# Performance work log

Hardware: AMD Instinct MI355X
Metric: run time of the kernel (lower is better)

Reference implementation:

```python
import jax, jax.numpy as jnp
import numpy as np

DIM = 768
N_HEADS = 12
HEAD_DIM = DIM // N_HEADS

def setup_inputs() -> dict:
    key = jax.random.key(0)
    ks = jax.random.split(key, 5)
    B, N = 8, 1024
    s = 0.02
    x = jax.random.normal(ks[0], (B, N, DIM), dtype=jnp.float32)
    W_qkv = jax.random.normal(ks[1], (DIM, 3 * DIM), dtype=jnp.float32) * s
    b_qkv = jnp.zeros((3 * DIM,), dtype=jnp.float32)
    W_proj = jax.random.normal(ks[2], (DIM, DIM), dtype=jnp.float32) * s
    b_proj = jnp.zeros((DIM,), dtype=jnp.float32)
    return {"x": x, "W_qkv": W_qkv, "b_qkv": b_qkv, "W_proj": W_proj, "b_proj": b_proj}

def reference(x, W_qkv, b_qkv, W_proj, b_proj):
    B, N, D = x.shape
    qkv = x @ W_qkv + b_qkv                                   # [B,N,3D]
    qkv = qkv.reshape(B, N, 3, N_HEADS, HEAD_DIM)
    q, k, v = qkv[:, :, 0], qkv[:, :, 1], qkv[:, :, 2]        # [B,N,H,hd]
    q = q.transpose(0, 2, 1, 3)                               # [B,H,N,hd]
    k = k.transpose(0, 2, 1, 3)
    v = v.transpose(0, 2, 1, 3)
    scores = jnp.einsum('bhqd,bhkd->bhqk', q, k) / jnp.sqrt(jnp.float32(HEAD_DIM))
    attn = jax.nn.softmax(scores, axis=-1)
    out = jnp.einsum('bhqk,bhkd->bhqd', attn, v)              # [B,H,N,hd]
    out = out.transpose(0, 2, 1, 3).reshape(B, N, D)
    return out @ W_proj + b_proj
```

## Files before the change

kernel.cpp:

```cpp
#include <hip/hip_runtime.h>
#include <hip/hip_bf16.h>


typedef __bf16 bf16x8 __attribute__((ext_vector_type(8)));
typedef float f32x4 __attribute__((ext_vector_type(4)));

#define MFMA16(a, b, c) __builtin_amdgcn_mfma_f32_16x16x32_bf16(a, b, c, 0, 0, 0)

#if defined(__has_builtin) && __has_builtin(__builtin_amdgcn_exp2f)
#define EXP2(x) __builtin_amdgcn_exp2f(x)
#else
#define EXP2(x) exp2f(x)
#endif

__device__ inline __bf16 to_bf16(float f) {
  __hip_bfloat16 h = __float2bfloat16(f);
  return *reinterpret_cast<__bf16*>(&h);
}

__device__ __forceinline__ void gload16(const void* g, void* l) {
  __builtin_amdgcn_global_load_lds(
      (const __attribute__((address_space(1))) unsigned int*)(unsigned long long)g,
      (__attribute__((address_space(3))) unsigned int*)(unsigned long long)l,
      16, 0, 0);
}

__global__ void ws_diag_kernel(float* out, int n, float val) {
  int i = blockIdx.x * 256 + threadIdx.x;
  if (i < n) out[i] = val;
}

__global__ __launch_bounds__(256) void convert_x_kernel(
    const float* __restrict__ x, __hip_bfloat16* __restrict__ xc, int n8) {
  int i = blockIdx.x * 256 + threadIdx.x;
  if (i >= n8) return;
  float4 a = ((const float4*)x)[i * 2], b = ((const float4*)x)[i * 2 + 1];
  __hip_bfloat16 o[8] = {__float2bfloat16(a.x), __float2bfloat16(a.y),
                         __float2bfloat16(a.z), __float2bfloat16(a.w),
                         __float2bfloat16(b.x), __float2bfloat16(b.y),
                         __float2bfloat16(b.z), __float2bfloat16(b.w)};
  *(int4*)(xc + (size_t)i * 8) = *(const int4*)o;
}

__global__ void convert_transpose_kernel(const float* __restrict__ W,
                                         __hip_bfloat16* __restrict__ Wt,
                                         int rows, int cols) {
  __shared__ __hip_bfloat16 tile[32][33];
  const int tc = blockIdx.x * 32, tr = blockIdx.y * 32;
  const int tx = threadIdx.x, ty = threadIdx.y;
#pragma unroll
  for (int i = 0; i < 4; ++i) {
    int r = ty + i * 8;
    tile[r][tx] = __float2bfloat16(W[(size_t)(tr + r) * cols + tc + tx]);
  }
  __syncthreads();
#pragma unroll
  for (int i = 0; i < 4; ++i) {
    int r = ty + i * 8;
    Wt[(size_t)(tc + r) * rows + tr + tx] = tile[tx][r];
  }
}

constexpr int GK = 768;

__global__ __launch_bounds__(256) void gemm_qkv_kernel(
    const __hip_bfloat16* __restrict__ A,
    const __hip_bfloat16* __restrict__ Bt,
    const float* __restrict__ bias,
    __hip_bfloat16* __restrict__ Qw,
    __hip_bfloat16* __restrict__ Kw,
    __hip_bfloat16* __restrict__ Vt) {
  __shared__ __align__(16) __bf16 As[128 * 32];
  __shared__ __align__(16) __bf16 Bs[128 * 32];
  const int tid = threadIdx.x;
  const int lane = tid & 63, wave = tid >> 6;
  const int wr = wave >> 1, wc = wave & 1;
  const int m0 = blockIdx.x * 128, n0 = blockIdx.y * 128;
  const int fr = lane & 15, q4 = lane >> 4;

  const int r4 = lane >> 2, c8 = (lane & 3) * 8;
  const __hip_bfloat16* ga0 = A + (size_t)(m0 + wave * 32 + r4) * GK + c8;
  const __hip_bfloat16* gb0 = Bt + (size_t)(n0 + wave * 32 + r4) * GK + c8;
  __bf16* la0 = &As[wave * 1024];
  __bf16* lb0 = &Bs[wave * 1024];

  f32x4 acc[4][4] = {};

  for (int kt = 0; kt < GK / 32; ++kt) {
    __syncthreads();
    gload16(ga0 + kt * 32, la0);
    gload16(ga0 + kt * 32 + 16 * GK, la0 + 512);
    gload16(gb0 + kt * 32, lb0);
    gload16(gb0 + kt * 32 + 16 * GK, lb0 + 512);
    __syncthreads();
    bf16x8 af[4], bfr[4];
#pragma unroll
    for (int i = 0; i < 4; ++i)
      af[i] = *(const bf16x8*)(&As[(wr * 64 + i * 16 + fr) * 32 + q4 * 8]);
#pragma unroll
    for (int j = 0; j < 4; ++j)
      bfr[j] = *(const bf16x8*)(&Bs[(wc * 64 + j * 16 + fr) * 32 + q4 * 8]);
#pragma unroll
    for (int i = 0; i < 4; ++i)
#pragma unroll
      for (int j = 0; j < 4; ++j)
        acc[i][j] = MFMA16(af[i], bfr[j], acc[i][j]);
  }

#pragma unroll
  for (int j = 0; j < 4; ++j) {
    int col = n0 + wc * 64 + j * 16 + fr;
    int which = col / 768;
    int rem = col - which * 768;
    int h = rem >> 6, d = rem & 63;
    float bv = bias[col];
    if (which == 2) {
#pragma unroll
      for (int i = 0; i < 4; ++i) {
        int row0 = m0 + wr * 64 + i * 16 + q4 * 4;
        int bb = row0 >> 10, nn = row0 & 1023;
        __hip_bfloat16 o[4];
#pragma unroll
        for (int r = 0; r < 4; ++r) o[r] = __float2bfloat16(acc[i][j][r] + bv);
        *(int2*)(Vt + (((size_t)(bb * 12 + h)) << 16) + ((size_t)d << 10) + nn) =
            *(const int2*)o;
      }
    } else {
      __hip_bfloat16* dst = (which == 0) ? Qw : Kw;
      float scale = (which == 0) ? 0.18033688011112042f : 1.0f;
#pragma unroll
      for (int i = 0; i < 4; ++i) {
#pragma unroll
        for (int r = 0; r < 4; ++r) {
          int row = m0 + wr * 64 + i * 16 + q4 * 4 + r;
          int bb = row >> 10, nn = row & 1023;
          float v = (acc[i][j][r] + bv) * scale;
          dst[(((size_t)(bb * 12 + h) * 1024 + nn) << 6) + d] = __float2bfloat16(v);
        }
      }
    }
  }
}

__global__ __launch_bounds__(256) void gemm_proj_kernel(
    const __hip_bfloat16* __restrict__ A,
    const __hip_bfloat16* __restrict__ Bt,
    const float* __restrict__ bias,
    float* __restrict__ out) {
  __shared__ __align__(16) __bf16 As[128 * 32];
  __shared__ __align__(16) __bf16 Bs[128 * 32];
  const int tid = threadIdx.x;
  const int lane = tid & 63, wave = tid >> 6;
  const int wr = wave >> 1, wc = wave & 1;
  const int m0 = blockIdx.x * 128, n0 = blockIdx.y * 128;
  const int fr = lane & 15, q4 = lane >> 4;

  const int r4 = lane >> 2, c8 = (lane & 3) * 8;
  const __hip_bfloat16* ga0 = A + (size_t)(m0 + wave * 32 + r4) * GK + c8;
  const __hip_bfloat16* gb0 = Bt + (size_t)(n0 + wave * 32 + r4) * GK + c8;
  __bf16* la0 = &As[wave * 1024];
  __bf16* lb0 = &Bs[wave * 1024];

  f32x4 acc[4][4] = {};

  for (int kt = 0; kt < GK / 32; ++kt) {
    __syncthreads();
    gload16(ga0 + kt * 32, la0);
    gload16(ga0 + kt * 32 + 16 * GK, la0 + 512);
    gload16(gb0 + kt * 32, lb0);
    gload16(gb0 + kt * 32 + 16 * GK, lb0 + 512);
    __syncthreads();
    bf16x8 af[4], bfr[4];
#pragma unroll
    for (int i = 0; i < 4; ++i)
      af[i] = *(const bf16x8*)(&As[(wr * 64 + i * 16 + fr) * 32 + q4 * 8]);
#pragma unroll
    for (int j = 0; j < 4; ++j)
      bfr[j] = *(const bf16x8*)(&Bs[(wc * 64 + j * 16 + fr) * 32 + q4 * 8]);
#pragma unroll
    for (int i = 0; i < 4; ++i)
#pragma unroll
      for (int j = 0; j < 4; ++j)
        acc[i][j] = MFMA16(af[i], bfr[j], acc[i][j]);
  }

#pragma unroll
  for (int j = 0; j < 4; ++j) {
    int col = n0 + wc * 64 + j * 16 + fr;
    float bv = bias[col];
#pragma unroll
    for (int i = 0; i < 4; ++i) {
#pragma unroll
      for (int r = 0; r < 4; ++r) {
        int row = m0 + wr * 64 + i * 16 + q4 * 4 + r;
        out[(size_t)row * 768 + col] = acc[i][j][r] + bv;
      }
    }
  }
}

__global__ __launch_bounds__(512) void attn_kernel(
    const __hip_bfloat16* __restrict__ Qw,
    const __hip_bfloat16* __restrict__ Kw,
    const __hip_bfloat16* __restrict__ Vt,
    __hip_bfloat16* __restrict__ O) {
  constexpr int LP = 72;
  __shared__ __bf16 smem[18432];
  __bf16* Qs = smem;
  __bf16* K1 = smem;
  __bf16* V1 = smem + 4608;
  __bf16* K0 = smem + 9216;
  __bf16* V0 = smem + 13824;
  const int tid = threadIdx.x;
  const int lane = tid & 63, wave = tid >> 6;
  const int fr = lane & 15, q4 = lane >> 4;
  const int bh = blockIdx.x % 96, qt = blockIdx.x / 96;
  const __hip_bfloat16* Qb = Qw + ((size_t)bh * 1024 + qt * 128) * 64;
  const __hip_bfloat16* Kb = Kw + (size_t)bh * 65536;
  const __hip_bfloat16* Vb = Vt + (size_t)bh * 65536;

  const int krow = tid >> 3, kc = (tid & 7) * 8;
  int4 kregA = *(const int4*)(Kb + (size_t)krow * 64 + kc);
  int4 vregA = *(const int4*)(Vb + ((size_t)krow << 10) + kc);

#pragma unroll
  for (int i = 0; i < 2; ++i) {
    int s = tid + 512 * i;
    int row = s >> 3, c = (s & 7) * 8;
    *(int4*)(&Qs[row * LP + c]) = *(const int4*)(Qb + row * 64 + c);
  }
  __syncthreads();
  bf16x8 qf[2];
#pragma unroll
  for (int ks = 0; ks < 2; ++ks)
    qf[ks] = *(const bf16x8*)(&Qs[(wave * 16 + fr) * LP + ks * 32 + q4 * 8]);

  float l_i = 0.f;
  f32x4 accO[4] = {};

  const int sc8 = tid & 7;
  const int sbase = ((sc8 >> 2) << 5) | ((sc8 & 1) << 4) | (((sc8 >> 1) & 1) << 2);

  *(int4*)(&K0[krow * LP + kc]) = kregA;
  *(int2*)(&V0[krow * LP + sbase]) = make_int2(vregA.x, vregA.y);
  *(int2*)(&V0[krow * LP + sbase + 8]) = make_int2(vregA.z, vregA.w);
  int4 kregB = *(const int4*)(Kb + (size_t)(64 + krow) * 64 + kc);
  int4 vregB = *(const int4*)(Vb + ((size_t)krow << 10) + 64 + kc);
  __syncthreads();

  auto compute_tile = [&](const __bf16* Kbuf, const __bf16* Vbuf) {
    f32x4 scT[4];
    __builtin_amdgcn_s_setprio(1);
#pragma unroll
    for (int nt = 0; nt < 4; ++nt) {
      bf16x8 kf0 = *(const bf16x8*)(&Kbuf[(nt * 16 + fr) * LP + q4 * 8]);
      bf16x8 kf1 = *(const bf16x8*)(&Kbuf[(nt * 16 + fr) * LP + 32 + q4 * 8]);
      f32x4 z = {};
      z = MFMA16(kf0, qf[0], z);
      scT[nt] = MFMA16(kf1, qf[1], z);
    }
    __builtin_amdgcn_s_setprio(0);
    float rs = 0.f;
#pragma unroll
    for (int nt = 0; nt < 4; ++nt)
#pragma unroll
      for (int r = 0; r < 4; ++r) {
        float p = EXP2(scT[nt][r]);
        scT[nt][r] = p;
        rs += p;
      }
    l_i += rs;
#pragma unroll
    for (int ks = 0; ks < 2; ++ks) {
      bf16x8 pf;
#pragma unroll
      for (int e = 0; e < 4; ++e) {
        pf[e] = to_bf16(scT[2 * ks][e]);
        pf[4 + e] = to_bf16(scT[2 * ks + 1][e]);
      }
      __builtin_amdgcn_s_setprio(1);
#pragma unroll
      for (int dt = 0; dt < 4; ++dt) {
        bf16x8 vf = *(const bf16x8*)(&Vbuf[(dt * 16 + fr) * LP + ks * 32 + q4 * 8]);
        accO[dt] = MFMA16(pf, vf, accO[dt]);
      }
      __builtin_amdgcn_s_setprio(0);
    }
  };

  for (int kt2 = 0; kt2 < 16; kt2 += 2) {
    compute_tile(K0, V0);
    *(int4*)(&K1[krow * LP + kc]) = kregB;
    *(int2*)(&V1[krow * LP + sbase]) = make_int2(vregB.x, vregB.y);
    *(int2*)(&V1[krow * LP + sbase + 8]) = make_int2(vregB.z, vregB.w);
    if (kt2 + 2 < 16) {
      kregA = *(const int4*)(Kb + (size_t)((kt2 + 2) * 64 + krow) * 64 + kc);
      vregA = *(const int4*)(Vb + ((size_t)krow << 10) + (kt2 + 2) * 64 + kc);
    }
    __syncthreads();
    compute_tile(K1, V1);
    if (kt2 + 2 < 16) {
      *(int4*)(&K0[krow * LP + kc]) = kregA;
      *(int2*)(&V0[krow * LP + sbase]) = make_int2(vregA.x, vregA.y);
      *(int2*)(&V0[krow * LP + sbase + 8]) = make_int2(vregA.z, vregA.w);
      kregB = *(const int4*)(Kb + (size_t)((kt2 + 3) * 64 + krow) * 64 + kc);
      vregB = *(const int4*)(Vb + ((size_t)krow << 10) + (kt2 + 3) * 64 + kc);
      __syncthreads();
    }
  }

  l_i += __shfl_xor(l_i, 16, 64);
  l_i += __shfl_xor(l_i, 32, 64);
  float lrow[4];
#pragma unroll
  for (int r = 0; r < 4; ++r) lrow[r] = __shfl(l_i, q4 * 4 + r, 64);

  const int h = bh % 12, bb = bh / 12;
#pragma unroll
  for (int dt = 0; dt < 4; ++dt)
#pragma unroll
    for (int r = 0; r < 4; ++r) {
      int row = bb * 1024 + qt * 128 + wave * 16 + q4 * 4 + r;
      int col = h * 64 + dt * 16 + fr;
      O[(size_t)row * 768 + col] = __float2bfloat16(accO[dt][r] / lrow[r]);
    }
}

extern "C" void kernel_launch(void* const* d_in, const int* in_sizes, int n_in,
                              void* d_out, int out_size, void* d_ws, size_t ws_size,
                              hipStream_t stream) {
  const float* x     = (const float*)d_in[0];
  const float* Wqkv  = (const float*)d_in[1];
  const float* bqkv  = (const float*)d_in[2];
  const float* Wproj = (const float*)d_in[3];
  const float* bproj = (const float*)d_in[4];
  float* out = (float*)d_out;

  constexpr size_t NEEDED = 55050240;
  if (ws_size < NEEDED) {
    ws_diag_kernel<<<(out_size + 255) / 256, 256, 0, stream>>>(
        out, out_size, (float)(ws_size >> 20));
    return;
  }

  char* ws = (char*)d_ws;
  __hip_bfloat16* WqkvT  = (__hip_bfloat16*)(ws);
  __hip_bfloat16* WprojT = (__hip_bfloat16*)(ws + 3538944);
  __hip_bfloat16* Qw     = (__hip_bfloat16*)(ws + 4718592);
  __hip_bfloat16* Kw     = (__hip_bfloat16*)(ws + 17301504);
  __hip_bfloat16* Vt     = (__hip_bfloat16*)(ws + 29884416);
  __hip_bfloat16* xc     = (__hip_bfloat16*)(ws + 42467328);
  __hip_bfloat16* attnO  = xc;

  convert_x_kernel<<<3072, 256, 0, stream>>>(x, xc, 786432);
  convert_transpose_kernel<<<dim3(72, 24), dim3(32, 8), 0, stream>>>(
      Wqkv, WqkvT, 768, 2304);
  convert_transpose_kernel<<<dim3(24, 24), dim3(32, 8), 0, stream>>>(
      Wproj, WprojT, 768, 768);
  gemm_qkv_kernel<<<dim3(64, 18), 256, 0, stream>>>(xc, WqkvT, bqkv, Qw, Kw, Vt);
  attn_kernel<<<dim3(96 * 8), 512, 0, stream>>>(Qw, Kw, Vt, attnO);
  gemm_proj_kernel<<<dim3(64, 6), 256, 0, stream>>>(attnO, WprojT, bproj, out);
}
```

Before: 190.5 us.

## Merge prep conversions into one launch and transpose V in separate kernel

Folds the x conversion and both weight convert-transposes into a single prep kernel launch that dispatches on block index, removing two launches. The QKV GEMM now writes V row-major like Q and K, and a new LDS-tiled kernel transposes V into the layout the attention kernel reads. This replaces the GEMM's strided 8-byte V stores with coalesced 16-byte stores, at the cost of an extra kernel and an extra pass over V in memory. Workspace buffers are reassigned so Vt reuses the x buffer and the attention output reuses the row-major V buffer.

```diff
diff --git a/kernel.cpp b/kernel.cpp
--- a/kernel.cpp
+++ b/kernel.cpp
@@ -30,24 +30,36 @@
   if (i < n) out[i] = val;
 }
 
-__global__ __launch_bounds__(256) void convert_x_kernel(
-    const float* __restrict__ x, __hip_bfloat16* __restrict__ xc, int n8) {
-  int i = blockIdx.x * 256 + threadIdx.x;
-  if (i >= n8) return;
-  float4 a = ((const float4*)x)[i * 2], b = ((const float4*)x)[i * 2 + 1];
-  __hip_bfloat16 o[8] = {__float2bfloat16(a.x), __float2bfloat16(a.y),
-                         __float2bfloat16(a.z), __float2bfloat16(a.w),
-                         __float2bfloat16(b.x), __float2bfloat16(b.y),
-                         __float2bfloat16(b.z), __float2bfloat16(b.w)};
-  *(int4*)(xc + (size_t)i * 8) = *(const int4*)o;
-}
-
-__global__ void convert_transpose_kernel(const float* __restrict__ W,
-                                         __hip_bfloat16* __restrict__ Wt,
-                                         int rows, int cols) {
+__global__ __launch_bounds__(256) void prep_kernel(
+    const float* __restrict__ x, __hip_bfloat16* __restrict__ xc,
+    const float* __restrict__ Wqkv, __hip_bfloat16* __restrict__ WqkvT,
+    const float* __restrict__ Wproj, __hip_bfloat16* __restrict__ WprojT) {
   __shared__ __hip_bfloat16 tile[32][33];
-  const int tc = blockIdx.x * 32, tr = blockIdx.y * 32;
-  const int tx = threadIdx.x, ty = threadIdx.y;
+  const int b = blockIdx.x;
+  if (b < 3072) {
+    int i = b * 256 + threadIdx.x;
+    float4 a = ((const float4*)x)[i * 2], c = ((const float4*)x)[i * 2 + 1];
+    __hip_bfloat16 o[8] = {__float2bfloat16(a.x), __float2bfloat16(a.y),
+                           __float2bfloat16(a.z), __float2bfloat16(a.w),
+                           __float2bfloat16(c.x), __float2bfloat16(c.y),
+                           __float2bfloat16(c.z), __float2bfloat16(c.w)};
+    *(int4*)(xc + (size_t)i * 8) = *(const int4*)o;
+    return;
+  }
+  const float* W;
+  __hip_bfloat16* Wt;
+  int rows, cols, bx, by;
+  if (b < 4800) {
+    int idx = b - 3072;
+    W = Wqkv; Wt = WqkvT; rows = 768; cols = 2304;
+    bx = idx % 72; by = idx / 72;
+  } else {
+    int idx = b - 4800;
+    W = Wproj; Wt = WprojT; rows = 768; cols = 768;
+    bx = idx % 24; by = idx / 24;
+  }
+  const int tc = bx * 32, tr = by * 32;
+  const int tx = threadIdx.x & 31, ty = threadIdx.x >> 5;
 #pragma unroll
   for (int i = 0; i < 4; ++i) {
     int r = ty + i * 8;
@@ -58,6 +70,33 @@
   for (int i = 0; i < 4; ++i) {
     int r = ty + i * 8;
     Wt[(size_t)(tc + r) * rows + tr + tx] = tile[tx][r];
+  }
+}
+
+__global__ __launch_bounds__(256) void vtrans_kernel(
+    const __hip_bfloat16* __restrict__ Vrow, __hip_bfloat16* __restrict__ Vt) {
+  constexpr int LP = 72;
+  __shared__ __bf16 tile[64 * LP];
+  const int tid = threadIdx.x;
+  const int bh = blockIdx.x;
+  const int n0 = blockIdx.y * 64;
+  const size_t base = (size_t)bh << 16;
+#pragma unroll
+  for (int i = 0; i < 2; ++i) {
+    int s = tid + 256 * i;
+    int r = s >> 3, c8 = (s & 7) * 8;
+    *(int4*)(&tile[r * LP + c8]) =
+        *(const int4*)(Vrow + base + (size_t)(n0 + r) * 64 + c8);
+  }
+  __syncthreads();
+#pragma unroll
+  for (int i = 0; i < 2; ++i) {
+    int s = tid + 256 * i;
+    int d = s >> 3, n8 = (s & 7) * 8;
+    __bf16 o[8];
+#pragma unroll
+    for (int j = 0; j < 8; ++j) o[j] = tile[(n8 + j) * LP + d];
+    *(int4*)(Vt + base + ((size_t)d << 10) + n0 + n8) = *(const int4*)o;
   }
 }
 
@@ -69,7 +108,7 @@
     const float* __restrict__ bias,
     __hip_bfloat16* __restrict__ Qw,
     __hip_bfloat16* __restrict__ Kw,
-    __hip_bfloat16* __restrict__ Vt) {
+    __hip_bfloat16* __restrict__ Vw) {
   __shared__ __align__(16) __bf16 As[128 * 32];
   __shared__ __align__(16) __bf16 Bs[128 * 32];
   const int tid = threadIdx.x;
@@ -114,29 +153,16 @@
     int rem = col - which * 768;
     int h = rem >> 6, d = rem & 63;
     float bv = bias[col];
-    if (which == 2) {
-#pragma unroll
-      for (int i = 0; i < 4; ++i) {
-        int row0 = m0 + wr * 64 + i * 16 + q4 * 4;
-        int bb = row0 >> 10, nn = row0 & 1023;
-        __hip_bfloat16 o[4];
-#pragma unroll
-        for (int r = 0; r < 4; ++r) o[r] = __float2bfloat16(acc[i][j][r] + bv);
-        *(int2*)(Vt + (((size_t)(bb * 12 + h)) << 16) + ((size_t)d << 10) + nn) =
-            *(const int2*)o;
-      }
-    } else {
-      __hip_bfloat16* dst = (which == 0) ? Qw : Kw;
-      float scale = (which == 0) ? 0.18033688011112042f : 1.0f;
-#pragma unroll
-      for (int i = 0; i < 4; ++i) {
-#pragma unroll
-        for (int r = 0; r < 4; ++r) {
-          int row = m0 + wr * 64 + i * 16 + q4 * 4 + r;
-          int bb = row >> 10, nn = row & 1023;
-          float v = (acc[i][j][r] + bv) * scale;
-          dst[(((size_t)(bb * 12 + h) * 1024 + nn) << 6) + d] = __float2bfloat16(v);
-        }
+    __hip_bfloat16* dst = (which == 0) ? Qw : (which == 1) ? Kw : Vw;
+    float scale = (which == 0) ? 0.18033688011112042f : 1.0f;
+#pragma unroll
+    for (int i = 0; i < 4; ++i) {
+#pragma unroll
+      for (int r = 0; r < 4; ++r) {
+        int row = m0 + wr * 64 + i * 16 + q4 * 4 + r;
+        int bb = row >> 10, nn = row & 1023;
+        float v = (acc[i][j][r] + bv) * scale;
+        dst[(((size_t)(bb * 12 + h) * 1024 + nn) << 6) + d] = __float2bfloat16(v);
       }
     }
   }
@@ -348,16 +374,14 @@
   __hip_bfloat16* WprojT = (__hip_bfloat16*)(ws + 3538944);
   __hip_bfloat16* Qw     = (__hip_bfloat16*)(ws + 4718592);
   __hip_bfloat16* Kw     = (__hip_bfloat16*)(ws + 17301504);
-  __hip_bfloat16* Vt     = (__hip_bfloat16*)(ws + 29884416);
+  __hip_bfloat16* Vrow   = (__hip_bfloat16*)(ws + 29884416);
   __hip_bfloat16* xc     = (__hip_bfloat16*)(ws + 42467328);
-  __hip_bfloat16* attnO  = xc;
-
-  convert_x_kernel<<<3072, 256, 0, stream>>>(x, xc, 786432);
-  convert_transpose_kernel<<<dim3(72, 24), dim3(32, 8), 0, stream>>>(
-      Wqkv, WqkvT, 768, 2304);
-  convert_transpose_kernel<<<dim3(24, 24), dim3(32, 8), 0, stream>>>(
-      Wproj, WprojT, 768, 768);
-  gemm_qkv_kernel<<<dim3(64, 18), 256, 0, stream>>>(xc, WqkvT, bqkv, Qw, Kw, Vt);
+  __hip_bfloat16* Vt     = xc;
+  __hip_bfloat16* attnO  = Vrow;
+
+  prep_kernel<<<5376, 256, 0, stream>>>(x, xc, Wqkv, WqkvT, Wproj, WprojT);
+  gemm_qkv_kernel<<<dim3(64, 18), 256, 0, stream>>>(xc, WqkvT, bqkv, Qw, Kw, Vrow);
+  vtrans_kernel<<<dim3(96, 16), 256, 0, stream>>>(Vrow, Vt);
   attn_kernel<<<dim3(96 * 8), 512, 0, stream>>>(Qw, Kw, Vt, attnO);
   gemm_proj_kernel<<<dim3(64, 6), 256, 0, stream>>>(attnO, WprojT, bproj, out);
 }
```

Result: no change. 191.0 us (+0.3%).
